# Optimization experiments

Measured on AMD Instinct MI355X. Metric: run time of the kernel, lower is better.

Reference implementation:

```python
import jax, jax.numpy as jnp
import numpy as np

T, B, IN, H, F, OUT = 2048, 32, 256, 512, 2048, 256


def setup_inputs() -> dict:
    key = jax.random.key(0)
    ks = jax.random.split(key, 9)
    s_in = 1.0 / np.sqrt(IN)
    s_h = 1.0 / np.sqrt(H)
    s_f = 1.0 / np.sqrt(F)
    return {
        "x": jax.random.normal(ks[0], (T, B, IN), dtype=jnp.float32),
        "Wg": jax.random.uniform(ks[1], (H, IN), jnp.float32, -s_in, s_in),
        "bg": jax.random.uniform(ks[2], (H,), jnp.float32, -s_in, s_in),
        "Wi": jax.random.uniform(ks[3], (H, IN), jnp.float32, -s_in, s_in),
        "bi": jax.random.uniform(ks[4], (H,), jnp.float32, -s_in, s_in),
        "W1": jax.random.uniform(ks[5], (F, H), jnp.float32, -s_h, s_h),
        "b1": jax.random.uniform(ks[6], (F,), jnp.float32, -s_h, s_h),
        "W2": jax.random.uniform(ks[7], (OUT, F), jnp.float32, -s_f, s_f),
        "b2": jax.random.uniform(ks[8], (OUT,), jnp.float32, -s_f, s_f),
    }


def _gilr_scan(a, b):
    # h_t = a_t * h_{t-1} + b_t with h_0 = 0  ->  parallel associative scan over time
    def combine(c1, c2):
        a1, b1 = c1
        a2, b2 = c2
        return (a1 * a2, b1 * a2 + b2)
    _, h = jax.lax.associative_scan(combine, (a, b), axis=0)
    return h


def reference(x, Wg, bg, Wi, bi, W1, b1, W2, b2):
    # x: (T, B, IN)
    g = jax.nn.sigmoid(jnp.einsum("tbi,hi->tbh", x, Wg) + bg)  # (T,B,H)
    i = jnp.tanh(jnp.einsum("tbi,hi->tbh", x, Wi) + bi)        # (T,B,H)
    h = _gilr_scan(g, (1.0 - g) * i)                             # (T,B,H)
    z = jax.nn.gelu(jnp.einsum("tbh,fh->tbf", h, W1) + b1, approximate=False)
    out = jnp.einsum("tbf,of->tbo", z, W2) + b2                  # (T,B,OUT)
    return out
```

## Files before the change

kernel.cpp:

```cpp
#include <hip/hip_runtime.h>
#include <hip/hip_fp16.h>
#include <math.h>


#define T_DIM 2048
#define B_DIM 32
#define IN_DIM 256
#define H_DIM 512
#define F_DIM 2048
#define OUT_DIM 256

typedef _Float16 f16;
typedef _Float16 f16x8 __attribute__((ext_vector_type(8)));
typedef float f32x4 __attribute__((ext_vector_type(4)));

#define AS3(p) ((__attribute__((address_space(3))) void*)(p))
#define AS1(p) ((const __attribute__((address_space(1))) void*)(p))
#define MFMA16(d, x, y) d = __builtin_amdgcn_mfma_f32_16x16x32_f16(x, y, d, 0, 0, 0)


__global__ void cvt_kernel(const float* __restrict__ in, f16* __restrict__ out, int n8) {
  int i = blockIdx.x * blockDim.x + threadIdx.x;
  if (i >= n8) return;
  const float4* p = (const float4*)in + (size_t)i * 2;
  float4 a = p[0], b = p[1];
  f16x8 o = { (f16)a.x, (f16)a.y, (f16)a.z, (f16)a.w,
              (f16)b.x, (f16)b.y, (f16)b.z, (f16)b.w };
  *((f16x8*)out + i) = o;
}

__global__ void bias_cat_kernel(const float* __restrict__ bg, const float* __restrict__ bi,
                                float* __restrict__ bgi) {
  int t = threadIdx.x;
  bgi[t] = (t < 512) ? bg[t] : bi[t - 512];
}

__device__ __forceinline__ float sigmoid_fast(float v) {
  return __builtin_amdgcn_rcpf(1.0f + __expf(-v));
}
__device__ __forceinline__ float tanh_fast(float v) {
  return 1.0f - 2.0f * __builtin_amdgcn_rcpf(__expf(2.0f * v) + 1.0f);
}
__device__ __forceinline__ float gelu_fast(float v) {
  float u = v * v;
  float y = v * fmaf(0.0713548353f, u, 1.59576912161f);
  return v * __builtin_amdgcn_rcpf(1.0f + __expf(-y));
}


__global__ __launch_bounds__(256, 2) void gemm1_k(
    const float* __restrict__ X, const f16* __restrict__ Bw,
    const float* __restrict__ bias, f16* __restrict__ Cout) {
  constexpr int NT = 4, LDA = 256, LDB = 256, LDC = 1024;
  __shared__ f16 lds[2][2][128][64];
  const int tid = threadIdx.x, wid = tid >> 6, lane = tid & 63;
  const int bid = blockIdx.x;
  const int m0 = ((bid & 7) * 64 + (bid >> 6)) * 128;
  const int n0 = ((bid >> 3) & 7) * 128;
  const int wr = (wid >> 1) * 64, wc = (wid & 1) * 64;

  float4 sa[4][2];
  auto loadA = [&](int kt) {
#pragma unroll
    for (int q = 0; q < 4; ++q) {
      int s = tid * 4 + q, row = s >> 3, c = s & 7;
      const float4* p = (const float4*)(X + (size_t)(m0 + row) * LDA + kt * 64 + c * 8);
      sa[q][0] = p[0]; sa[q][1] = p[1];
    }
  };
  auto writeA = [&](int buf) {
#pragma unroll
    for (int q = 0; q < 4; ++q) {
      int s = tid * 4 + q, row = s >> 3, c = s & 7;
      float4 a = sa[q][0], b = sa[q][1];
      f16x8 o = { (f16)a.x, (f16)a.y, (f16)a.z, (f16)a.w,
                  (f16)b.x, (f16)b.y, (f16)b.z, (f16)b.w };
      *(f16x8*)&lds[buf][0][row][c * 8] = o;
    }
  };
  auto stageB = [&](int buf, int kt) {
    const f16* gb = Bw + (size_t)n0 * LDB + kt * 64;
    f16* lb = &lds[buf][1][0][0];
#pragma unroll
    for (int q = 0; q < 4; ++q) {
      int seg = (wid << 2) + q;
      int s2 = seg * 64 + lane;
      int row = s2 >> 3, col = (s2 & 7) << 3;
      __builtin_amdgcn_global_load_lds(AS1(gb + (size_t)row * LDB + col),
                                       AS3(lb + seg * 512), 16, 0, 0);
    }
  };

  f32x4 acc[4][4] = {};
  loadA(0); writeA(0); stageB(0, 0);
  for (int kt = 0; kt < NT; ++kt) {
    __syncthreads();
    if (kt + 1 < NT) { loadA(kt + 1); stageB((kt + 1) & 1, kt + 1); }
    f16(*At)[64] = lds[kt & 1][0];
    f16(*Bt)[64] = lds[kt & 1][1];
    const int r = lane & 15, cg = (lane >> 4) << 3;
#pragma unroll
    for (int kk = 0; kk < 2; ++kk) {
      f16x8 af[4], bf[4];
#pragma unroll
      for (int i = 0; i < 4; ++i)
        af[i] = *(const f16x8*)&At[wr + i * 16 + r][kk * 32 + cg];
#pragma unroll
      for (int i = 0; i < 4; ++i)
        bf[i] = *(const f16x8*)&Bt[wc + i * 16 + r][kk * 32 + cg];
#pragma unroll
      for (int mi = 0; mi < 4; ++mi)
#pragma unroll
        for (int ni = 0; ni < 4; ++ni)
          MFMA16(acc[mi][ni], af[mi], bf[ni]);
    }
    if (kt + 1 < NT) writeA((kt + 1) & 1);
  }

  __syncthreads();
  f16* ep = &lds[0][0][0][0] + wid * 4096;
  const int r = lane & 15, rq = (lane >> 4) * 4;
#pragma unroll
  for (int ni = 0; ni < 4; ++ni) {
    int gcol = n0 + wc + ni * 16 + r;
    float bv = bias[gcol];
    bool sig = gcol < 512;
    int cc = ni * 2 + (r >> 3);
#pragma unroll
    for (int mi = 0; mi < 4; ++mi) {
#pragma unroll
      for (int j = 0; j < 4; ++j) {
        int lrow = mi * 16 + rq + j;
        float v = acc[mi][ni][j] + bv;
        float av = sig ? sigmoid_fast(v) : tanh_fast(v);
        ep[lrow * 64 + ((cc ^ (lrow & 7)) << 3) + (r & 7)] = (f16)av;
      }
    }
  }
  asm volatile("s_waitcnt lgkmcnt(0)" ::: "memory");
  __builtin_amdgcn_sched_barrier(0);
#pragma unroll
  for (int t = 0; t < 8; ++t) {
    int idx = t * 64 + lane;
    int row = idx >> 3, c = idx & 7;
    f16x8 v = *(const f16x8*)(ep + row * 64 + ((c ^ (row & 7)) << 3));
    *(f16x8*)(Cout + (size_t)(m0 + wr + row) * LDC + n0 + wc + c * 8) = v;
  }
}


__global__ __launch_bounds__(256, 4) void gemm2_tlp(
    const f16* __restrict__ A, const f16* __restrict__ Bw,
    const float* __restrict__ bias, f16* __restrict__ Cout) {
  constexpr int LDA = 1024, LDB = 512, LDC = 2048, NT = 16;
  __shared__ f16 lds[2][2][128][32];
  const int tid = threadIdx.x, wid = tid >> 6, lane = tid & 63;
  const int bid = blockIdx.x;
  const int m0 = ((bid & 7) * 16 + (bid >> 7)) * 128;
  const int n0 = ((bid >> 3) & 15) * 128;
  const int wr = (wid >> 1) * 64, wc = (wid & 1) * 64;

  const f16* srcA[2]; const f16* srcB[2];
#pragma unroll
  for (int q = 0; q < 2; ++q) {
    int s = (wid * 2 + q) * 64 + lane;
    int row = s >> 2, g = (s & 3) ^ ((row >> 1) & 3);
    srcA[q] = A + (size_t)(m0 + row) * LDA + g * 8;
    srcB[q] = Bw + (size_t)(n0 + row) * LDB + g * 8;
  }
  auto stage = [&](int buf, int kt) {
    f16* la = &lds[buf][0][0][0] + (wid * 2) * 512;
    f16* lb = &lds[buf][1][0][0] + (wid * 2) * 512;
#pragma unroll
    for (int q = 0; q < 2; ++q) {
      __builtin_amdgcn_global_load_lds(AS1(srcA[q] + kt * 32), AS3(la + q * 512), 16, 0, 0);
      __builtin_amdgcn_global_load_lds(AS1(srcB[q] + kt * 32), AS3(lb + q * 512), 16, 0, 0);
    }
  };
  const int r = lane & 15;
  const int cs = (((lane >> 4) ^ ((lane >> 1) & 3)) << 3);

  f32x4 acc[4][4] = {};
  stage(0, 0);
  for (int kt = 0; kt < NT; ++kt) {
    __syncthreads();
    if (kt + 1 < NT) stage((kt + 1) & 1, kt + 1);
    f16(*At)[32] = lds[kt & 1][0];
    f16(*Bt)[32] = lds[kt & 1][1];
    f16x8 af[4], bf[4];
#pragma unroll
    for (int i = 0; i < 4; ++i) af[i] = *(const f16x8*)&At[wr + i * 16 + r][cs];
#pragma unroll
    for (int i = 0; i < 4; ++i) bf[i] = *(const f16x8*)&Bt[wc + i * 16 + r][cs];
#pragma unroll
    for (int mi = 0; mi < 4; ++mi)
#pragma unroll
      for (int ni = 0; ni < 4; ++ni)
        MFMA16(acc[mi][ni], af[mi], bf[ni]);
  }

  __syncthreads();
  f16* ep = &lds[0][0][0][0] + wid * 4096;
  const int rq = (lane >> 4) * 4;
#pragma unroll
  for (int ni = 0; ni < 4; ++ni) {
    float bv = bias[n0 + wc + ni * 16 + r];
    int cc = ni * 2 + (r >> 3);
#pragma unroll
    for (int mi = 0; mi < 4; ++mi) {
#pragma unroll
      for (int j = 0; j < 4; ++j) {
        int lrow = mi * 16 + rq + j;
        float v = gelu_fast(acc[mi][ni][j] + bv);
        ep[lrow * 64 + ((cc ^ (lrow & 7)) << 3) + (r & 7)] = (f16)v;
      }
    }
  }
  asm volatile("s_waitcnt lgkmcnt(0)" ::: "memory");
  __builtin_amdgcn_sched_barrier(0);
#pragma unroll
  for (int t = 0; t < 8; ++t) {
    int idx = t * 64 + lane;
    int row = idx >> 3, c = idx & 7;
    f16x8 v = *(const f16x8*)(ep + row * 64 + ((c ^ (row & 7)) << 3));
    *(f16x8*)(Cout + (size_t)(m0 + wr + row) * LDC + n0 + wc + c * 8) = v;
  }
}


__global__ __launch_bounds__(256, 2) void gemm2_f(
    const f16* __restrict__ A, const f16* __restrict__ Bw,
    const float* __restrict__ bias, f16* __restrict__ Cout) {
  constexpr int LDA = 1024, LDB = 512, LDC = 2048, NT = 16;
  __shared__ f16 lds[3][384 * 32];
  const int tid = threadIdx.x, wid = tid >> 6, lane = tid & 63;
  const int lr = lane & 15;
  const int bid = blockIdx.x;
  const int m0 = ((bid & 7) * 8 + (bid >> 7)) * 256;
  const int n0 = ((bid >> 3) & 15) * 128;
  const int wr = (wid >> 1) * 128, wc = (wid & 1) * 64;

  const f16* srcA[4];
  const f16* srcB[2];
#pragma unroll
  for (int q = 0; q < 4; ++q) {
    int s = wid * 256 + q * 64 + lane;
    int row = s >> 2, g = (s & 3) ^ ((row + (row >> 2)) & 3);
    srcA[q] = A + (size_t)(m0 + row) * LDA + g * 8;
  }
#pragma unroll
  for (int q = 0; q < 2; ++q) {
    int s = wid * 128 + q * 64 + lane;
    int row = s >> 2, g = (s & 3) ^ ((row + (row >> 2)) & 3);
    srcB[q] = Bw + (size_t)(n0 + row) * LDB + g * 8;
  }
  auto stageA = [&](int buf, int kt) {
    f16* d = lds[buf] + wid * 2048;
#pragma unroll
    for (int q = 0; q < 4; ++q)
      __builtin_amdgcn_global_load_lds(AS1(srcA[q] + kt * 32), AS3(d + q * 512), 16, 0, 0);
  };
  auto stageB = [&](int buf, int kt) {
    f16* d = lds[buf] + 8192 + wid * 1024;
#pragma unroll
    for (int q = 0; q < 2; ++q)
      __builtin_amdgcn_global_load_lds(AS1(srcB[q] + kt * 32), AS3(d + q * 512), 16, 0, 0);
  };
  const int qsf = (((lane >> 4) ^ ((lr + (lr >> 2)) & 3)) << 3);
  auto fragA = [&](int buf, int mi) -> f16x8 {
    return *(const f16x8*)(lds[buf] + (wr + mi * 16 + lr) * 32 + qsf);
  };
  auto fragB = [&](int buf, int ni) -> f16x8 {
    return *(const f16x8*)(lds[buf] + 8192 + (wc + ni * 16 + lr) * 32 + qsf);
  };

  f32x4 acc[8][4] = {};
  stageA(0, 0); stageB(0, 0);
  stageA(1, 1); stageB(1, 1);
  asm volatile("s_waitcnt vmcnt(6)" ::: "memory");
  __builtin_amdgcn_s_barrier();

#pragma unroll
  for (int kt = 0; kt < NT; ++kt) {
    const int cur = kt % 3, nx2 = (kt + 2) % 3;
    f16x8 a[8], b[4];
#pragma unroll
    for (int mi = 0; mi < 8; ++mi) a[mi] = fragA(cur, mi);
#pragma unroll
    for (int ni = 0; ni < 4; ++ni) b[ni] = fragB(cur, ni);
    if (kt + 2 < NT) { stageA(nx2, kt + 2); stageB(nx2, kt + 2); }
    asm volatile("s_waitcnt lgkmcnt(0)" ::: "memory");
    __builtin_amdgcn_sched_barrier(0);
    __builtin_amdgcn_s_setprio(1);
#pragma unroll
    for (int mi = 0; mi < 8; ++mi) {
      MFMA16(acc[mi][0], a[mi], b[0]); MFMA16(acc[mi][1], a[mi], b[1]);
      MFMA16(acc[mi][2], a[mi], b[2]); MFMA16(acc[mi][3], a[mi], b[3]);
    }
    __builtin_amdgcn_s_setprio(0);
    if (kt + 2 < NT) asm volatile("s_waitcnt vmcnt(6)" ::: "memory");
    else             asm volatile("s_waitcnt vmcnt(0)" ::: "memory");
    __builtin_amdgcn_s_barrier();
  }

  __syncthreads();
  f16* ep = &lds[0][0] + wid * 8192;
  const int rq = (lane >> 4) * 4;
#pragma unroll
  for (int mi = 0; mi < 8; ++mi) {
#pragma unroll
    for (int ni = 0; ni < 4; ++ni) {
      int c = ni * 2 + (lr >> 3);
      float bv = bias[n0 + wc + ni * 16 + lr];
#pragma unroll
      for (int j = 0; j < 4; ++j) {
        int row = mi * 16 + rq + j;
        float v = gelu_fast(acc[mi][ni][j] + bv);
        ep[row * 64 + ((c ^ (row & 7)) << 3) + (lr & 7)] = (f16)v;
      }
    }
  }
  asm volatile("s_waitcnt lgkmcnt(0)" ::: "memory");
  __builtin_amdgcn_sched_barrier(0);
#pragma unroll
  for (int t = 0; t < 16; ++t) {
    int idx = t * 64 + lane;
    int row = idx >> 3, c = idx & 7;
    f16x8 v = *(const f16x8*)(ep + row * 64 + ((c ^ (row & 7)) << 3));
    *(f16x8*)(Cout + (size_t)(m0 + wr + row) * LDC + (n0 + wc) + c * 8) = v;
  }
}


__global__ __launch_bounds__(256, 2) void gemm3_k(
    const f16* __restrict__ A, const f16* __restrict__ Bw,
    const float* __restrict__ bias, float* __restrict__ Cout) {
  constexpr int LDA = 2048, LDB = 2048, LDC = 256, NT = 32;
  __shared__ f16 lds[2][2][128][64];
  const int tid = threadIdx.x, wid = tid >> 6, lane = tid & 63;
  const int bid = blockIdx.x;
  const int m0 = ((bid & 7) * 16 + (bid >> 4)) * 128;
  const int n0 = ((bid >> 3) & 1) * 128;
  const int wr = (wid >> 1) * 64, wc = (wid & 1) * 64;

  auto stage = [&](int buf, int kt) {
    const f16* ga = A + (size_t)m0 * LDA + kt * 64;
    const f16* gb = Bw + (size_t)n0 * LDB + kt * 64;
    f16* la = &lds[buf][0][0][0];
    f16* lb = &lds[buf][1][0][0];
#pragma unroll
    for (int q = 0; q < 4; ++q) {
      int seg = (wid << 2) + q;
      int s = seg * 64 + lane;
      int row = s >> 3, col = (s & 7) << 3;
      __builtin_amdgcn_global_load_lds(AS1(ga + (size_t)row * LDA + col),
                                       AS3(la + seg * 512), 16, 0, 0);
      __builtin_amdgcn_global_load_lds(AS1(gb + (size_t)row * LDB + col),
                                       AS3(lb + seg * 512), 16, 0, 0);
    }
  };

  f32x4 acc[4][4] = {};
  stage(0, 0);
  for (int kt = 0; kt < NT; ++kt) {
    __syncthreads();
    if (kt + 1 < NT) stage((kt + 1) & 1, kt + 1);
    f16(*At)[64] = lds[kt & 1][0];
    f16(*Bt)[64] = lds[kt & 1][1];
    const int r = lane & 15, cg = (lane >> 4) << 3;
#pragma unroll
    for (int kk = 0; kk < 2; ++kk) {
      f16x8 af[4], bf[4];
#pragma unroll
      for (int i = 0; i < 4; ++i)
        af[i] = *(const f16x8*)&At[wr + i * 16 + r][kk * 32 + cg];
#pragma unroll
      for (int i = 0; i < 4; ++i)
        bf[i] = *(const f16x8*)&Bt[wc + i * 16 + r][kk * 32 + cg];
#pragma unroll
      for (int mi = 0; mi < 4; ++mi)
#pragma unroll
        for (int ni = 0; ni < 4; ++ni)
          MFMA16(acc[mi][ni], af[mi], bf[ni]);
    }
  }
  const int r = lane & 15, rq = (lane >> 4) * 4;
#pragma unroll
  for (int ni = 0; ni < 4; ++ni) {
    int col = n0 + wc + ni * 16 + r;
    float bv = bias[col];
#pragma unroll
    for (int mi = 0; mi < 4; ++mi) {
#pragma unroll
      for (int j = 0; j < 4; ++j) {
        int row = m0 + wr + mi * 16 + rq + j;
        Cout[(size_t)row * LDC + col] = acc[mi][ni][j] + bv;
      }
    }
  }
}


#define NCH 16384
#define NCHUNK 32
#define CLEN 64

__global__ void scan_p1(const f16* __restrict__ ab, float* __restrict__ cA,
                        float* __restrict__ cH) {
  int ch = blockIdx.x * 256 + threadIdx.x;
  int c = blockIdx.y;
  const f16* pg = ab + (size_t)(c * CLEN) * 32768 + (ch >> 9) * 1024 + (ch & 511);
  const f16* pi = pg + 512;
  float A = 1.f, Hl = 0.f;
  for (int t = 0; t < CLEN; ++t) {
    float g = (float)pg[0];
    float ii = (float)pi[0];
    Hl = fmaf(g, Hl - ii, ii);
    A *= g;
    pg += 32768; pi += 32768;
  }
  cA[c * NCH + ch] = A;
  cH[c * NCH + ch] = Hl;
}

__global__ void scan_p2(const float* __restrict__ cA, const float* __restrict__ cH,
                        float* __restrict__ st) {
  int ch = blockIdx.x * 256 + threadIdx.x;
  float h0 = 0.f;
  for (int c = 0; c < NCHUNK; ++c) {
    st[c * NCH + ch] = h0;
    h0 = cA[c * NCH + ch] * h0 + cH[c * NCH + ch];
  }
}

__global__ void scan_p3(f16* __restrict__ ab, const float* __restrict__ st) {
  int ch = blockIdx.x * 256 + threadIdx.x;
  int c = blockIdx.y;
  f16* pg = ab + (size_t)(c * CLEN) * 32768 + (ch >> 9) * 1024 + (ch & 511);
  const f16* pi = pg + 512;
  float hv = st[c * NCH + ch];
  for (int t = 0; t < CLEN; ++t) {
    float g = (float)pg[0];
    float ii = (float)pi[0];
    hv = fmaf(g, hv - ii, ii);
    pg[0] = (f16)hv;
    pg += 32768; pi += 32768;
  }
}


extern "C" void kernel_launch(void* const* d_in, const int* in_sizes, int n_in,
                              void* d_out, int out_size, void* d_ws, size_t ws_size,
                              hipStream_t stream) {
  const float* x  = (const float*)d_in[0];
  const float* Wg = (const float*)d_in[1];
  const float* bg = (const float*)d_in[2];
  const float* Wi = (const float*)d_in[3];
  const float* bi = (const float*)d_in[4];
  const float* W1 = (const float*)d_in[5];
  const float* b1 = (const float*)d_in[6];
  const float* W2 = (const float*)d_in[7];
  const float* b2 = (const float*)d_in[8];
  float* out = (float*)d_out;

  char* ws = (char*)d_ws;
  f16*   wgi16 = (f16*)(ws + 0);
  f16*   w116  = (f16*)(ws + 524288);
  f16*   w216  = (f16*)(ws + 2621440);
  float* bgi   = (float*)(ws + 3670016);
  f16*   ab16  = (f16*)(ws + 37748736);
  float* cA    = (float*)(ws + 171966464);
  float* cH    = (float*)(ws + 174063616);
  float* st    = (float*)(ws + 176160768);
  f16*   z16   = (f16*)(ws + 178257920);
  if (ws_size < 245366784) return;

  cvt_kernel<<<64, 256, 0, stream>>>(Wg, wgi16, 16384);
  cvt_kernel<<<64, 256, 0, stream>>>(Wi, wgi16 + 131072, 16384);
  cvt_kernel<<<512, 256, 0, stream>>>(W1, w116, 131072);
  cvt_kernel<<<256, 256, 0, stream>>>(W2, w216, 65536);
  bias_cat_kernel<<<1, 1024, 0, stream>>>(bg, bi, bgi);

  gemm1_k<<<4096, 256, 0, stream>>>(x, wgi16, bgi, ab16);

  scan_p1<<<dim3(64, NCHUNK), 256, 0, stream>>>(ab16, cA, cH);
  scan_p2<<<64, 256, 0, stream>>>(cA, cH, st);
  scan_p3<<<dim3(64, NCHUNK), 256, 0, stream>>>(ab16, st);

  for (int s = 0; s < 4; ++s) {
    const f16* hs = ab16 + (size_t)s * 16384 * 1024;
    if (s < 2)
      gemm2_tlp<<<2048, 256, 0, stream>>>(hs, w116, b1, z16);
    else
      gemm2_f<<<1024, 256, 0, stream>>>(hs, w116, b1, z16);
    gemm3_k<<<256, 256, 0, stream>>>(z16, w216, b2, out + (size_t)s * 16384 * 256);
  }
}
```

Measured before the change: 563.0 us.

## Enlarge gemm1 tiles to 256x128 and unify gemm2 into one double-buffered kernel

gemm1 now computes 256x128 output tiles with a K-step of 32 and an XOR-swizzled LDS layout, halving the grid and giving each wave twice as many MFMA accumulators per fragment load. The two gemm2 variants (the small-tile TLP kernel used for the first two slices and the triple-buffered 256-row kernel used for the rest) are replaced by one 256x128 double-buffered kernel with a simpler swizzle, used for all four slices. The epilogues are split into two halves so the per-wave staging buffer stays small. Giving up triple buffering, the manual vmcnt waits and the setprio hints in gemm2 may expose more load latency, and larger tiles raise register pressure.

New measurement: 509.5 us. -9.5%, faster.

```diff
diff --git a/kernel.cpp b/kernel.cpp
--- a/kernel.cpp
+++ b/kernel.cpp
@@ -3,8 +3,6 @@
 #include <math.h>
 
 
-#define T_DIM 2048
-#define B_DIM 32
 #define IN_DIM 256
 #define H_DIM 512
 #define F_DIM 2048
@@ -51,190 +49,120 @@
 __global__ __launch_bounds__(256, 2) void gemm1_k(
     const float* __restrict__ X, const f16* __restrict__ Bw,
     const float* __restrict__ bias, f16* __restrict__ Cout) {
-  constexpr int NT = 4, LDA = 256, LDB = 256, LDC = 1024;
-  __shared__ f16 lds[2][2][128][64];
+  constexpr int LDB = 256, LDC = 1024, NT = 8;
+  __shared__ f16 lds[24576];
   const int tid = threadIdx.x, wid = tid >> 6, lane = tid & 63;
+  const int r = lane & 15;
   const int bid = blockIdx.x;
-  const int m0 = ((bid & 7) * 64 + (bid >> 6)) * 128;
+  const int m0 = ((bid & 7) * 32 + (bid >> 6)) * 256;
   const int n0 = ((bid >> 3) & 7) * 128;
-  const int wr = (wid >> 1) * 64, wc = (wid & 1) * 64;
+  const int wr = (wid >> 1) * 128, wc = (wid & 1) * 64;
+
+  int aoff[4];
+#pragma unroll
+  for (int q = 0; q < 4; ++q) {
+    int s = wid * 256 + q * 64 + lane;
+    int row = s >> 2, g = (s & 3) ^ ((row >> 1) & 3);
+    aoff[q] = (m0 + row) * IN_DIM + g * 8;
+  }
+  const f16* srcB[2];
+#pragma unroll
+  for (int q = 0; q < 2; ++q) {
+    int s = wid * 128 + q * 64 + lane;
+    int row = s >> 2, g = (s & 3) ^ ((row >> 1) & 3);
+    srcB[q] = Bw + (size_t)(n0 + row) * LDB + g * 8;
+  }
 
   float4 sa[4][2];
   auto loadA = [&](int kt) {
 #pragma unroll
     for (int q = 0; q < 4; ++q) {
-      int s = tid * 4 + q, row = s >> 3, c = s & 7;
-      const float4* p = (const float4*)(X + (size_t)(m0 + row) * LDA + kt * 64 + c * 8);
+      const float4* p = (const float4*)(X + (size_t)aoff[q] + kt * 32);
       sa[q][0] = p[0]; sa[q][1] = p[1];
     }
   };
   auto writeA = [&](int buf) {
 #pragma unroll
     for (int q = 0; q < 4; ++q) {
-      int s = tid * 4 + q, row = s >> 3, c = s & 7;
       float4 a = sa[q][0], b = sa[q][1];
       f16x8 o = { (f16)a.x, (f16)a.y, (f16)a.z, (f16)a.w,
                   (f16)b.x, (f16)b.y, (f16)b.z, (f16)b.w };
-      *(f16x8*)&lds[buf][0][row][c * 8] = o;
+      *(f16x8*)(lds + buf * 8192 + wid * 2048 + q * 512 + lane * 8) = o;
     }
   };
   auto stageB = [&](int buf, int kt) {
-    const f16* gb = Bw + (size_t)n0 * LDB + kt * 64;
-    f16* lb = &lds[buf][1][0][0];
-#pragma unroll
-    for (int q = 0; q < 4; ++q) {
-      int seg = (wid << 2) + q;
-      int s2 = seg * 64 + lane;
-      int row = s2 >> 3, col = (s2 & 7) << 3;
-      __builtin_amdgcn_global_load_lds(AS1(gb + (size_t)row * LDB + col),
-                                       AS3(lb + seg * 512), 16, 0, 0);
-    }
+#pragma unroll
+    for (int q = 0; q < 2; ++q)
+      __builtin_amdgcn_global_load_lds(AS1(srcB[q] + kt * 32),
+          AS3(lds + 16384 + buf * 4096 + wid * 1024 + q * 512), 16, 0, 0);
   };
 
-  f32x4 acc[4][4] = {};
+  const int xorc = (((lane >> 4) ^ ((r >> 1) & 3)) << 3);
+  f32x4 acc[8][4] = {};
   loadA(0); writeA(0); stageB(0, 0);
   for (int kt = 0; kt < NT; ++kt) {
+    const int cur = kt & 1, nb = cur ^ 1;
     __syncthreads();
-    if (kt + 1 < NT) { loadA(kt + 1); stageB((kt + 1) & 1, kt + 1); }
-    f16(*At)[64] = lds[kt & 1][0];
-    f16(*Bt)[64] = lds[kt & 1][1];
-    const int r = lane & 15, cg = (lane >> 4) << 3;
-#pragma unroll
-    for (int kk = 0; kk < 2; ++kk) {
-      f16x8 af[4], bf[4];
-#pragma unroll
-      for (int i = 0; i < 4; ++i)
-        af[i] = *(const f16x8*)&At[wr + i * 16 + r][kk * 32 + cg];
-#pragma unroll
-      for (int i = 0; i < 4; ++i)
-        bf[i] = *(const f16x8*)&Bt[wc + i * 16 + r][kk * 32 + cg];
-#pragma unroll
-      for (int mi = 0; mi < 4; ++mi)
-#pragma unroll
-        for (int ni = 0; ni < 4; ++ni)
-          MFMA16(acc[mi][ni], af[mi], bf[ni]);
-    }
-    if (kt + 1 < NT) writeA((kt + 1) & 1);
+    if (kt + 1 < NT) { loadA(kt + 1); stageB(nb, kt + 1); }
+    f16x8 af[8], bf[4];
+#pragma unroll
+    for (int mi = 0; mi < 8; ++mi)
+      af[mi] = *(const f16x8*)(lds + cur * 8192 + (wr + mi * 16 + r) * 32 + xorc);
+#pragma unroll
+    for (int ni = 0; ni < 4; ++ni)
+      bf[ni] = *(const f16x8*)(lds + 16384 + cur * 4096 + (wc + ni * 16 + r) * 32 + xorc);
+#pragma unroll
+    for (int mi = 0; mi < 8; ++mi)
+#pragma unroll
+      for (int ni = 0; ni < 4; ++ni)
+        MFMA16(acc[mi][ni], af[mi], bf[ni]);
+    if (kt + 1 < NT) writeA(nb);
   }
 
   __syncthreads();
-  f16* ep = &lds[0][0][0][0] + wid * 4096;
-  const int r = lane & 15, rq = (lane >> 4) * 4;
-#pragma unroll
-  for (int ni = 0; ni < 4; ++ni) {
-    int gcol = n0 + wc + ni * 16 + r;
-    float bv = bias[gcol];
-    bool sig = gcol < 512;
-    int cc = ni * 2 + (r >> 3);
+  f16* ep = lds + wid * 4096;
+  const int rq = (lane >> 4) * 4;
+#pragma unroll
+  for (int h = 0; h < 2; ++h) {
 #pragma unroll
     for (int mi = 0; mi < 4; ++mi) {
 #pragma unroll
-      for (int j = 0; j < 4; ++j) {
-        int lrow = mi * 16 + rq + j;
-        float v = acc[mi][ni][j] + bv;
-        float av = sig ? sigmoid_fast(v) : tanh_fast(v);
-        ep[lrow * 64 + ((cc ^ (lrow & 7)) << 3) + (r & 7)] = (f16)av;
+      for (int ni = 0; ni < 4; ++ni) {
+        int gcol = n0 + wc + ni * 16 + r;
+        float bv = bias[gcol];
+        bool sig = gcol < 512;
+        int cc = ni * 2 + (r >> 3);
+#pragma unroll
+        for (int j = 0; j < 4; ++j) {
+          int lrow = mi * 16 + rq + j;
+          float v = acc[h * 4 + mi][ni][j] + bv;
+          float av = sig ? sigmoid_fast(v) : tanh_fast(v);
+          ep[lrow * 64 + ((cc ^ (lrow & 7)) << 3) + (r & 7)] = (f16)av;
+        }
       }
     }
-  }
-  asm volatile("s_waitcnt lgkmcnt(0)" ::: "memory");
-  __builtin_amdgcn_sched_barrier(0);
-#pragma unroll
-  for (int t = 0; t < 8; ++t) {
-    int idx = t * 64 + lane;
-    int row = idx >> 3, c = idx & 7;
-    f16x8 v = *(const f16x8*)(ep + row * 64 + ((c ^ (row & 7)) << 3));
-    *(f16x8*)(Cout + (size_t)(m0 + wr + row) * LDC + n0 + wc + c * 8) = v;
-  }
-}
-
-
-__global__ __launch_bounds__(256, 4) void gemm2_tlp(
+    asm volatile("s_waitcnt lgkmcnt(0)" ::: "memory");
+    __builtin_amdgcn_sched_barrier(0);
+#pragma unroll
+    for (int t = 0; t < 8; ++t) {
+      int idx = t * 64 + lane;
+      int row = idx >> 3, c = idx & 7;
+      f16x8 v = *(const f16x8*)(ep + row * 64 + ((c ^ (row & 7)) << 3));
+      *(f16x8*)(Cout + (size_t)(m0 + wr + h * 64 + row) * LDC + n0 + wc + c * 8) = v;
+    }
+    asm volatile("s_waitcnt lgkmcnt(0)" ::: "memory");
+    __builtin_amdgcn_sched_barrier(0);
+  }
+}
+
+
+__global__ __launch_bounds__(256, 2) void gemm2_k(
     const f16* __restrict__ A, const f16* __restrict__ Bw,
     const float* __restrict__ bias, f16* __restrict__ Cout) {
   constexpr int LDA = 1024, LDB = 512, LDC = 2048, NT = 16;
-  __shared__ f16 lds[2][2][128][32];
+  __shared__ f16 lds[24576];
   const int tid = threadIdx.x, wid = tid >> 6, lane = tid & 63;
-  const int bid = blockIdx.x;
-  const int m0 = ((bid & 7) * 16 + (bid >> 7)) * 128;
-  const int n0 = ((bid >> 3) & 15) * 128;
-  const int wr = (wid >> 1) * 64, wc = (wid & 1) * 64;
-
-  const f16* srcA[2]; const f16* srcB[2];
-#pragma unroll
-  for (int q = 0; q < 2; ++q) {
-    int s = (wid * 2 + q) * 64 + lane;
-    int row = s >> 2, g = (s & 3) ^ ((row >> 1) & 3);
-    srcA[q] = A + (size_t)(m0 + row) * LDA + g * 8;
-    srcB[q] = Bw + (size_t)(n0 + row) * LDB + g * 8;
-  }
-  auto stage = [&](int buf, int kt) {
-    f16* la = &lds[buf][0][0][0] + (wid * 2) * 512;
-    f16* lb = &lds[buf][1][0][0] + (wid * 2) * 512;
-#pragma unroll
-    for (int q = 0; q < 2; ++q) {
-      __builtin_amdgcn_global_load_lds(AS1(srcA[q] + kt * 32), AS3(la + q * 512), 16, 0, 0);
-      __builtin_amdgcn_global_load_lds(AS1(srcB[q] + kt * 32), AS3(lb + q * 512), 16, 0, 0);
-    }
-  };
   const int r = lane & 15;
-  const int cs = (((lane >> 4) ^ ((lane >> 1) & 3)) << 3);
-
-  f32x4 acc[4][4] = {};
-  stage(0, 0);
-  for (int kt = 0; kt < NT; ++kt) {
-    __syncthreads();
-    if (kt + 1 < NT) stage((kt + 1) & 1, kt + 1);
-    f16(*At)[32] = lds[kt & 1][0];
-    f16(*Bt)[32] = lds[kt & 1][1];
-    f16x8 af[4], bf[4];
-#pragma unroll
-    for (int i = 0; i < 4; ++i) af[i] = *(const f16x8*)&At[wr + i * 16 + r][cs];
-#pragma unroll
-    for (int i = 0; i < 4; ++i) bf[i] = *(const f16x8*)&Bt[wc + i * 16 + r][cs];
-#pragma unroll
-    for (int mi = 0; mi < 4; ++mi)
-#pragma unroll
-      for (int ni = 0; ni < 4; ++ni)
-        MFMA16(acc[mi][ni], af[mi], bf[ni]);
-  }
-
-  __syncthreads();
-  f16* ep = &lds[0][0][0][0] + wid * 4096;
-  const int rq = (lane >> 4) * 4;
-#pragma unroll
-  for (int ni = 0; ni < 4; ++ni) {
-    float bv = bias[n0 + wc + ni * 16 + r];
-    int cc = ni * 2 + (r >> 3);
-#pragma unroll
-    for (int mi = 0; mi < 4; ++mi) {
-#pragma unroll
-      for (int j = 0; j < 4; ++j) {
-        int lrow = mi * 16 + rq + j;
-        float v = gelu_fast(acc[mi][ni][j] + bv);
-        ep[lrow * 64 + ((cc ^ (lrow & 7)) << 3) + (r & 7)] = (f16)v;
-      }
-    }
-  }
-  asm volatile("s_waitcnt lgkmcnt(0)" ::: "memory");
-  __builtin_amdgcn_sched_barrier(0);
-#pragma unroll
-  for (int t = 0; t < 8; ++t) {
-    int idx = t * 64 + lane;
-    int row = idx >> 3, c = idx & 7;
-    f16x8 v = *(const f16x8*)(ep + row * 64 + ((c ^ (row & 7)) << 3));
-    *(f16x8*)(Cout + (size_t)(m0 + wr + row) * LDC + n0 + wc + c * 8) = v;
-  }
-}
-
-
-__global__ __launch_bounds__(256, 2) void gemm2_f(
-    const f16* __restrict__ A, const f16* __restrict__ Bw,
-    const float* __restrict__ bias, f16* __restrict__ Cout) {
-  constexpr int LDA = 1024, LDB = 512, LDC = 2048, NT = 16;
-  __shared__ f16 lds[3][384 * 32];
-  const int tid = threadIdx.x, wid = tid >> 6, lane = tid & 63;
-  const int lr = lane & 15;
   const int bid = blockIdx.x;
   const int m0 = ((bid & 7) * 8 + (bid >> 7)) * 256;
   const int n0 = ((bid >> 3) & 15) * 128;
@@ -245,89 +173,77 @@
 #pragma unroll
   for (int q = 0; q < 4; ++q) {
     int s = wid * 256 + q * 64 + lane;
-    int row = s >> 2, g = (s & 3) ^ ((row + (row >> 2)) & 3);
+    int row = s >> 2, g = (s & 3) ^ ((row >> 1) & 3);
     srcA[q] = A + (size_t)(m0 + row) * LDA + g * 8;
   }
 #pragma unroll
   for (int q = 0; q < 2; ++q) {
     int s = wid * 128 + q * 64 + lane;
-    int row = s >> 2, g = (s & 3) ^ ((row + (row >> 2)) & 3);
+    int row = s >> 2, g = (s & 3) ^ ((row >> 1) & 3);
     srcB[q] = Bw + (size_t)(n0 + row) * LDB + g * 8;
   }
-  auto stageA = [&](int buf, int kt) {
-    f16* d = lds[buf] + wid * 2048;
+  auto stage = [&](int buf, int kt) {
 #pragma unroll
     for (int q = 0; q < 4; ++q)
-      __builtin_amdgcn_global_load_lds(AS1(srcA[q] + kt * 32), AS3(d + q * 512), 16, 0, 0);
+      __builtin_amdgcn_global_load_lds(AS1(srcA[q] + kt * 32),
+          AS3(lds + buf * 8192 + wid * 2048 + q * 512), 16, 0, 0);
+#pragma unroll
+    for (int q = 0; q < 2; ++q)
+      __builtin_amdgcn_global_load_lds(AS1(srcB[q] + kt * 32),
+          AS3(lds + 16384 + buf * 4096 + wid * 1024 + q * 512), 16, 0, 0);
   };
-  auto stageB = [&](int buf, int kt) {
-    f16* d = lds[buf] + 8192 + wid * 1024;
-#pragma unroll
-    for (int q = 0; q < 2; ++q)
-      __builtin_amdgcn_global_load_lds(AS1(srcB[q] + kt * 32), AS3(d + q * 512), 16, 0, 0);
-  };
-  const int qsf = (((lane >> 4) ^ ((lr + (lr >> 2)) & 3)) << 3);
-  auto fragA = [&](int buf, int mi) -> f16x8 {
-    return *(const f16x8*)(lds[buf] + (wr + mi * 16 + lr) * 32 + qsf);
-  };
-  auto fragB = [&](int buf, int ni) -> f16x8 {
-    return *(const f16x8*)(lds[buf] + 8192 + (wc + ni * 16 + lr) * 32 + qsf);
-  };
-
+
+  const int xorc = (((lane >> 4) ^ ((r >> 1) & 3)) << 3);
   f32x4 acc[8][4] = {};
-  stageA(0, 0); stageB(0, 0);
-  stageA(1, 1); stageB(1, 1);
-  asm volatile("s_waitcnt vmcnt(6)" ::: "memory");
-  __builtin_amdgcn_s_barrier();
-
-#pragma unroll
+  stage(0, 0);
   for (int kt = 0; kt < NT; ++kt) {
-    const int cur = kt % 3, nx2 = (kt + 2) % 3;
-    f16x8 a[8], b[4];
-#pragma unroll
-    for (int mi = 0; mi < 8; ++mi) a[mi] = fragA(cur, mi);
-#pragma unroll
-    for (int ni = 0; ni < 4; ++ni) b[ni] = fragB(cur, ni);
-    if (kt + 2 < NT) { stageA(nx2, kt + 2); stageB(nx2, kt + 2); }
+    const int cur = kt & 1;
+    __syncthreads();
+    if (kt + 1 < NT) stage(cur ^ 1, kt + 1);
+    f16x8 af[8], bf[4];
+#pragma unroll
+    for (int mi = 0; mi < 8; ++mi)
+      af[mi] = *(const f16x8*)(lds + cur * 8192 + (wr + mi * 16 + r) * 32 + xorc);
+#pragma unroll
+    for (int ni = 0; ni < 4; ++ni)
+      bf[ni] = *(const f16x8*)(lds + 16384 + cur * 4096 + (wc + ni * 16 + r) * 32 + xorc);
+#pragma unroll
+    for (int mi = 0; mi < 8; ++mi)
+#pragma unroll
+      for (int ni = 0; ni < 4; ++ni)
+        MFMA16(acc[mi][ni], af[mi], bf[ni]);
+  }
+
+  __syncthreads();
+  f16* ep = lds + wid * 4096;
+  const int rq = (lane >> 4) * 4;
+#pragma unroll
+  for (int h = 0; h < 2; ++h) {
+#pragma unroll
+    for (int mi = 0; mi < 4; ++mi) {
+#pragma unroll
+      for (int ni = 0; ni < 4; ++ni) {
+        float bv = bias[n0 + wc + ni * 16 + r];
+        int cc = ni * 2 + (r >> 3);
+#pragma unroll
+        for (int j = 0; j < 4; ++j) {
+          int lrow = mi * 16 + rq + j;
+          float v = gelu_fast(acc[h * 4 + mi][ni][j] + bv);
+          ep[lrow * 64 + ((cc ^ (lrow & 7)) << 3) + (r & 7)] = (f16)v;
+        }
+      }
+    }
     asm volatile("s_waitcnt lgkmcnt(0)" ::: "memory");
     __builtin_amdgcn_sched_barrier(0);
-    __builtin_amdgcn_s_setprio(1);
-#pragma unroll
-    for (int mi = 0; mi < 8; ++mi) {
-      MFMA16(acc[mi][0], a[mi], b[0]); MFMA16(acc[mi][1], a[mi], b[1]);
-      MFMA16(acc[mi][2], a[mi], b[2]); MFMA16(acc[mi][3], a[mi], b[3]);
-    }
-    __builtin_amdgcn_s_setprio(0);
-    if (kt + 2 < NT) asm volatile("s_waitcnt vmcnt(6)" ::: "memory");
-    else             asm volatile("s_waitcnt vmcnt(0)" ::: "memory");
-    __builtin_amdgcn_s_barrier();
-  }
-
-  __syncthreads();
-  f16* ep = &lds[0][0] + wid * 8192;
-  const int rq = (lane >> 4) * 4;
-#pragma unroll
-  for (int mi = 0; mi < 8; ++mi) {
-#pragma unroll
-    for (int ni = 0; ni < 4; ++ni) {
-      int c = ni * 2 + (lr >> 3);
-      float bv = bias[n0 + wc + ni * 16 + lr];
-#pragma unroll
-      for (int j = 0; j < 4; ++j) {
-        int row = mi * 16 + rq + j;
-        float v = gelu_fast(acc[mi][ni][j] + bv);
-        ep[row * 64 + ((c ^ (row & 7)) << 3) + (lr & 7)] = (f16)v;
-      }
-    }
-  }
-  asm volatile("s_waitcnt lgkmcnt(0)" ::: "memory");
-  __builtin_amdgcn_sched_barrier(0);
-#pragma unroll
-  for (int t = 0; t < 16; ++t) {
-    int idx = t * 64 + lane;
-    int row = idx >> 3, c = idx & 7;
-    f16x8 v = *(const f16x8*)(ep + row * 64 + ((c ^ (row & 7)) << 3));
-    *(f16x8*)(Cout + (size_t)(m0 + wr + row) * LDC + (n0 + wc) + c * 8) = v;
+#pragma unroll
+    for (int t = 0; t < 8; ++t) {
+      int idx = t * 64 + lane;
+      int row = idx >> 3, c = idx & 7;
+      f16x8 v = *(const f16x8*)(ep + row * 64 + ((c ^ (row & 7)) << 3));
+      *(f16x8*)(Cout + (size_t)(m0 + wr + h * 64 + row) * LDC + n0 + wc + c * 8) = v;
+    }
+    asm volatile("s_waitcnt lgkmcnt(0)" ::: "memory");
+    __builtin_amdgcn_sched_barrier(0);
   }
 }
 
@@ -481,7 +397,7 @@
   cvt_kernel<<<256, 256, 0, stream>>>(W2, w216, 65536);
   bias_cat_kernel<<<1, 1024, 0, stream>>>(bg, bi, bgi);
 
-  gemm1_k<<<4096, 256, 0, stream>>>(x, wgi16, bgi, ab16);
+  gemm1_k<<<2048, 256, 0, stream>>>(x, wgi16, bgi, ab16);
 
   scan_p1<<<dim3(64, NCHUNK), 256, 0, stream>>>(ab16, cA, cH);
   scan_p2<<<64, 256, 0, stream>>>(cA, cH, st);
@@ -489,10 +405,7 @@
 
   for (int s = 0; s < 4; ++s) {
     const f16* hs = ab16 + (size_t)s * 16384 * 1024;
-    if (s < 2)
-      gemm2_tlp<<<2048, 256, 0, stream>>>(hs, w116, b1, z16);
-    else
-      gemm2_f<<<1024, 256, 0, stream>>>(hs, w116, b1, z16);
+    gemm2_k<<<1024, 256, 0, stream>>>(hs, w116, b1, z16);
     gemm3_k<<<256, 256, 0, stream>>>(z16, w216, b2, out + (size_t)s * 16384 * 256);
   }
 }
```
